# Optimization experiments

Hardware: AMD Instinct MI355X
Metric: run time of the kernel (lower is better)

The kernel has to match this reference:

```python
import jax, jax.numpy as jnp
import numpy as np
from jax import lax

FAST_ITERATIONS = 100
INPUT_DIM = 1024
OUTPUT_DIM = 512
BATCH = 16384


def setup_inputs() -> dict:
    key = jax.random.key(0)
    kx, kw, km = jax.random.split(key, 3)
    x = jax.random.normal(kx, (BATCH, INPUT_DIM), dtype=jnp.float32)
    # Xavier-uniform init for W [output_dim, input_dim]
    limit = float(np.sqrt(6.0 / (INPUT_DIM + OUTPUT_DIM)))
    W = jax.random.uniform(kw, (OUTPUT_DIM, INPUT_DIM), dtype=jnp.float32,
                           minval=-limit, maxval=limit)
    # M is zero at init in the module; use a small random M (spectral radius ~0.45)
    # so the fixed-point iteration is stable and non-trivial.
    M = 0.02 * jax.random.normal(km, (OUTPUT_DIM, OUTPUT_DIM), dtype=jnp.float32)
    return {"x": x, "W": W, "M": M}


def reference(x, W, M):
    # y_init = x @ W.T; then 100 steps of y = Wx - y @ M (all coords use old y)
    Wx = x @ W.T  # [batch, output_dim]

    def step(y, _):
        return Wx - y @ M, None

    y, _ = lax.scan(step, Wx, None, length=FAST_ITERATIONS)
    return y
```

## Files before the change

kernel.cpp:

```cpp
#include <hip/hip_runtime.h>

typedef float f32x4 __attribute__((ext_vector_type(4)));
typedef __bf16 bf16x8 __attribute__((ext_vector_type(8)));
typedef unsigned short u16x4 __attribute__((ext_vector_type(4)));
typedef unsigned short u16x8 __attribute__((ext_vector_type(8)));

__device__ __forceinline__ unsigned short f2b(float f){
  return __builtin_bit_cast(unsigned short, (__bf16)f);
}
__device__ __forceinline__ float b2f(unsigned short u){
  union { unsigned x; float f; } v; v.x = ((unsigned)u) << 16; return v.f;
}
__device__ __forceinline__ void mfma3(f32x4& acc, bf16x8 ah, bf16x8 al, bf16x8 bh, bf16x8 bl){
  acc = __builtin_amdgcn_mfma_f32_16x16x32_bf16(ah, bh, acc, 0, 0, 0);
  acc = __builtin_amdgcn_mfma_f32_16x16x32_bf16(ah, bl, acc, 0, 0, 0);
  acc = __builtin_amdgcn_mfma_f32_16x16x32_bf16(al, bh, acc, 0, 0, 0);
}
__device__ __forceinline__ void gload16(const void* g, void* l){
  __builtin_amdgcn_global_load_lds((const __attribute__((address_space(1))) void*)g,
                                   (__attribute__((address_space(3))) void*)l, 16, 0, 0);
}

template<bool ATR>
__device__ __forceinline__ void loadA(const float* __restrict__ A, int i0, int k0,
                                      int tid, float* aR){
  if (ATR){
    int r32 = tid & 31, kg = tid >> 5;
    #pragma unroll
    for (int q = 0; q < 8; ++q)
      aR[q] = -A[(k0 + kg*8 + q)*512 + i0 + r32];
  } else {
    #pragma unroll
    for (int j = 0; j < 2; ++j){
      int p = tid + j*256;
      int row = p >> 4, kq = p & 15;
      f32x4 v = *reinterpret_cast<const f32x4*>(A + (i0+row)*512 + k0 + kq*4);
      #pragma unroll
      for (int e = 0; e < 4; ++e) aR[j*4+e] = v[e];
    }
  }
}
template<bool ATR>
__device__ __forceinline__ void writeA(const float* aR, int tid,
                                       unsigned short* Ah, unsigned short* Al){
  if (ATR){
    int r32 = tid & 31, kg = tid >> 5;
    #pragma unroll
    for (int q4 = 0; q4 < 2; ++q4){
      u16x4 hi, lo;
      #pragma unroll
      for (int e = 0; e < 4; ++e){
        float f = aR[q4*4+e];
        unsigned short h = f2b(f);
        hi[e] = h; lo[e] = f2b(f - b2f(h));
      }
      int off = r32*128 + (((kg*8 + q4*4)*2) ^ ((r32 & 7) << 4));
      *reinterpret_cast<u16x4*>((char*)Ah + off) = hi;
      *reinterpret_cast<u16x4*>((char*)Al + off) = lo;
    }
  } else {
    #pragma unroll
    for (int j = 0; j < 2; ++j){
      int p = tid + j*256;
      int row = p >> 4, kq = p & 15;
      u16x4 hi, lo;
      #pragma unroll
      for (int e = 0; e < 4; ++e){
        float f = aR[j*4+e];
        unsigned short h = f2b(f);
        hi[e] = h; lo[e] = f2b(f - b2f(h));
      }
      int off = row*128 + ((kq*8) ^ ((row & 7) << 4));
      *reinterpret_cast<u16x4*>((char*)Ah + off) = hi;
      *reinterpret_cast<u16x4*>((char*)Al + off) = lo;
    }
  }
}
template<bool BROWM>
__device__ __forceinline__ void loadB(const float* __restrict__ B, int j0, int k0,
                                      int sb, int tid, float* bR){
  if (BROWM){
    #pragma unroll
    for (int j = 0; j < 4; ++j){
      int p = tid + j*256;
      int n = p >> 4, kq = p & 15;
      f32x4 v = *reinterpret_cast<const f32x4*>(B + (j0+n)*512 + k0 + kq*4);
      #pragma unroll
      for (int e = 0; e < 4; ++e) bR[j*4+e] = -v[e];
    }
  } else {
    int n = tid & 63, kg = tid >> 6;
    #pragma unroll
    for (int q = 0; q < 16; ++q)
      bR[q] = B[(k0 + kg*16 + q)*sb + j0 + n];
  }
}
template<bool BROWM>
__device__ __forceinline__ void writeB(const float* bR, int tid,
                                       unsigned short* Bh, unsigned short* Bl){
  if (BROWM){
    #pragma unroll
    for (int j = 0; j < 4; ++j){
      int p = tid + j*256;
      int n = p >> 4, kq = p & 15;
      u16x4 hi, lo;
      #pragma unroll
      for (int e = 0; e < 4; ++e){
        float f = bR[j*4+e];
        unsigned short h = f2b(f);
        hi[e] = h; lo[e] = f2b(f - b2f(h));
      }
      int off = n*128 + ((kq*8) ^ ((n & 7) << 4));
      *reinterpret_cast<u16x4*>((char*)Bh + off) = hi;
      *reinterpret_cast<u16x4*>((char*)Bl + off) = lo;
    }
  } else {
    int n = tid & 63, kg = tid >> 6;
    #pragma unroll
    for (int q4 = 0; q4 < 4; ++q4){
      u16x4 hi, lo;
      #pragma unroll
      for (int e = 0; e < 4; ++e){
        float f = bR[q4*4+e];
        unsigned short h = f2b(f);
        hi[e] = h; lo[e] = f2b(f - b2f(h));
      }
      int off = n*128 + (((kg*16 + q4*4)*2) ^ ((n & 7) << 4));
      *reinterpret_cast<u16x4*>((char*)Bh + off) = hi;
      *reinterpret_cast<u16x4*>((char*)Bl + off) = lo;
    }
  }
}

template<bool ATR, bool BROWM, bool HASD, bool BFOUT>
__device__ __forceinline__ void gtile(
    const float* __restrict__ A, const float* __restrict__ B,
    const float* __restrict__ D, float* __restrict__ Cf,
    unsigned short* __restrict__ Cb, int i0, int j0, int sb, int so,
    unsigned short* Ah, unsigned short* Al,
    unsigned short* Bh, unsigned short* Bl, int tid)
{
  int lane = tid & 63, wave = tid >> 6;
  int wm = wave >> 1, wn = wave & 1;
  f32x4 acc[2] = {};
  float aR0[8], bR0[16], aR1[8], bR1[16];
  loadA<ATR>(A, i0, 0, tid, aR0);
  loadB<BROWM>(B, j0, 0, sb, tid, bR0);
  loadA<ATR>(A, i0, 64, tid, aR1);
  loadB<BROWM>(B, j0, 64, sb, tid, bR1);

#define CHAIN_MFMA_PHASE                                                   \
    { _Pragma("unroll")                                                    \
      for (int kk = 0; kk < 2; ++kk){                                      \
        int kb = (kk*32 + (lane >> 4)*8) * 2;                              \
        int arow = wm*16 + (lane & 15);                                    \
        int aoff = arow*128 + (kb ^ ((arow & 7) << 4));                    \
        bf16x8 ah = *reinterpret_cast<const bf16x8*>((char*)Ah + aoff);    \
        bf16x8 al = *reinterpret_cast<const bf16x8*>((char*)Al + aoff);    \
        _Pragma("unroll")                                                  \
        for (int n = 0; n < 2; ++n){                                       \
          int brow = wn*32 + n*16 + (lane & 15);                           \
          int boff = brow*128 + (kb ^ ((brow & 7) << 4));                  \
          bf16x8 bh = *reinterpret_cast<const bf16x8*>((char*)Bh + boff);  \
          bf16x8 bl = *reinterpret_cast<const bf16x8*>((char*)Bl + boff);  \
          mfma3(acc[n], ah, al, bh, bl);                                   \
        }                                                                  \
      } }

  #pragma unroll 1
  for (int k0 = 0; k0 < 512; k0 += 128){
    writeA<ATR>(aR0, tid, Ah, Al);
    writeB<BROWM>(bR0, tid, Bh, Bl);
    __syncthreads();
    if (k0 + 128 < 512){
      loadA<ATR>(A, i0, k0 + 128, tid, aR0);
      loadB<BROWM>(B, j0, k0 + 128, sb, tid, bR0);
    }
    CHAIN_MFMA_PHASE
    __syncthreads();
    writeA<ATR>(aR1, tid, Ah, Al);
    writeB<BROWM>(bR1, tid, Bh, Bl);
    __syncthreads();
    if (k0 + 192 < 512){
      loadA<ATR>(A, i0, k0 + 192, tid, aR1);
      loadB<BROWM>(B, j0, k0 + 192, sb, tid, bR1);
    }
    CHAIN_MFMA_PHASE
    __syncthreads();
  }
#undef CHAIN_MFMA_PHASE

  #pragma unroll
  for (int n = 0; n < 2; ++n)
    #pragma unroll
    for (int r = 0; r < 4; ++r){
      int i = i0 + wm*16 + (lane >> 4)*4 + r;
      int j = j0 + wn*32 + n*16 + (lane & 15);
      float v = acc[n][r];
      if (HASD) v += D[i*so + j];
      if (BFOUT) Cb[i*so + j] = f2b(v);
      else       Cf[i*so + j] = v;
    }
}

__global__ __launch_bounds__(256, 2) void k_step(
    const float* __restrict__ Q, const float* __restrict__ R,
    float* __restrict__ Qout, float* __restrict__ Rout,
    unsigned short* __restrict__ Tout,
    const float* __restrict__ X, unsigned short* __restrict__ Xb,
    int first, int last, int convbase, int convend)
{
  __shared__ unsigned short Ah[32*64], Al[32*64], Bh[64*64], Bl[64*64];
  int tid = threadIdx.x, bid = blockIdx.x;
  int qend = last ? 256 : 384;
  if (bid < 256){
    int i0 = (bid >> 4) * 32, j0 = (bid & 15) * 64;
    if (last)
      gtile<false,false,true ,true >(Q, R, R, nullptr, Tout, i0, j0, 1024, 1024, Ah,Al,Bh,Bl, tid);
    else if (first)
      gtile<true ,false,true ,false>(Q, R, R, Rout, nullptr, i0, j0, 1024, 1024, Ah,Al,Bh,Bl, tid);
    else
      gtile<false,false,true ,false>(Q, R, R, Rout, nullptr, i0, j0, 1024, 1024, Ah,Al,Bh,Bl, tid);
  } else if (bid < qend){
    int t = bid - 256;
    int i0 = (t >> 3) * 32, j0 = (t & 7) * 64;
    if (first)
      gtile<true ,true ,false,false>(Q, Q, nullptr, Qout, nullptr, i0, j0, 512, 512, Ah,Al,Bh,Bl, tid);
    else
      gtile<false,false,false,false>(Q, Q, nullptr, Qout, nullptr, i0, j0, 512, 512, Ah,Al,Bh,Bl, tid);
  } else {
    for (int g = convbase + (bid - qend); g < convend; g += 128){
      const float* src = X + (size_t)g * 8192;
      unsigned short* dst = Xb + (size_t)g * 8192;
      #pragma unroll
      for (int it = 0; it < 8; ++it){
        int p = (tid + it*256) * 4;
        f32x4 v = *reinterpret_cast<const f32x4*>(src + p);
        u16x4 h;
        #pragma unroll
        for (int e = 0; e < 4; ++e) h[e] = f2b(v[e]);
        *reinterpret_cast<u16x4*>(dst + p) = h;
      }
    }
  }
}

__global__ __launch_bounds__(512, 1) void k_gemm10(const unsigned short* __restrict__ Xb,
                                                   const unsigned short* __restrict__ Tt,
                                                   float* __restrict__ Y)
{
  __shared__ unsigned short As_[2][128*64];
  __shared__ unsigned short Bs_[2][256*64];
  int tid = threadIdx.x;
  int lane = tid & 63, wave = tid >> 6;
  int wm = wave >> 2, wn = wave & 3;
  int bid = blockIdx.x;
  int wg = (bid & 7) * 32 + (bid >> 3);
  int m0 = (wg >> 1) * 128;
  int n0 = (wg & 1) * 256;

  int lrow = lane >> 3;
  int lg   = (lane & 7) ^ lrow;
  f32x4 acc[4][4] = {};

  #define STAGE(buf, kt)                                                         \
    { _Pragma("unroll")                                                          \
      for (int it = 0; it < 2; ++it){                                            \
        int r = wave*16 + it*8 + lrow;                                           \
        gload16((const void*)(Xb + (size_t)(m0 + r)*1024 + (kt)*64 + lg*8),      \
                (void*)&As_[buf][(wave*16 + it*8)*64]);                          \
      }                                                                          \
      _Pragma("unroll")                                                          \
      for (int it = 0; it < 4; ++it){                                            \
        int r = wave*32 + it*8 + lrow;                                           \
        gload16((const void*)(Tt + (size_t)(n0 + r)*1024 + (kt)*64 + lg*8),      \
                (void*)&Bs_[buf][(wave*32 + it*8)*64]);                          \
      } }

  STAGE(0, 0);
  STAGE(1, 1);
  #pragma unroll 1
  for (int kt = 0; kt < 16; ++kt){
    if (kt < 15) asm volatile("s_waitcnt vmcnt(6)" ::: "memory");
    else         asm volatile("s_waitcnt vmcnt(0)" ::: "memory");
    __builtin_amdgcn_s_barrier();
    const unsigned short* Ab = &As_[kt & 1][0];
    const unsigned short* Bb = &Bs_[kt & 1][0];
    #pragma unroll
    for (int kk = 0; kk < 2; ++kk){
      int gb = kk*4 + (lane >> 4);
      bf16x8 af[4], bfr[4];
      #pragma unroll
      for (int m = 0; m < 4; ++m){
        int row = wm*64 + m*16 + (lane & 15);
        af[m] = *reinterpret_cast<const bf16x8*>((char*)Ab + row*128 + ((gb ^ (row & 7))*16));
      }
      #pragma unroll
      for (int n = 0; n < 4; ++n){
        int row = wn*64 + n*16 + (lane & 15);
        bfr[n] = *reinterpret_cast<const bf16x8*>((char*)Bb + row*128 + ((gb ^ (row & 7))*16));
      }
      #pragma unroll
      for (int m = 0; m < 4; ++m)
        #pragma unroll
        for (int n = 0; n < 4; ++n)
          acc[m][n] = __builtin_amdgcn_mfma_f32_16x16x32_bf16(af[m], bfr[n], acc[m][n], 0,0,0);
    }
    __builtin_amdgcn_s_barrier();
    if (kt < 14) STAGE(kt & 1, kt + 2);
  }
  #undef STAGE

  #pragma unroll
  for (int m = 0; m < 4; ++m)
    #pragma unroll
    for (int n = 0; n < 4; ++n)
      #pragma unroll
      for (int r = 0; r < 4; ++r){
        int row = m0 + wm*64 + m*16 + (lane >> 4)*4 + r;
        int col = n0 + wn*64 + n*16 + (lane & 15);
        Y[(size_t)row*512 + col] = acc[m][n][r];
      }
}

extern "C" void kernel_launch(void* const* d_in, const int* in_sizes, int n_in,
                              void* d_out, int out_size, void* d_ws, size_t ws_size,
                              hipStream_t stream) {
  const float* x = (const float*)d_in[0];
  const float* W = (const float*)d_in[1];
  const float* M = (const float*)d_in[2];
  float* y = (float*)d_out;

  float* Qa = (float*)d_ws;
  float* Qb = Qa + 512*512;
  float* Ra = Qb + 512*512;
  float* Rb = Ra + 512*1024;
  unsigned short* Tt = (unsigned short*)(Rb + 512*1024);
  unsigned short* Xb = Tt + 512*1024;

  k_step<<<512, 256, 0, stream>>>(M,  W,  Qa, Ra, nullptr, x, Xb, 1, 0,    0,  512);
  k_step<<<512, 256, 0, stream>>>(Qa, Ra, Qb, Rb, nullptr, x, Xb, 0, 0,  512, 1024);
  k_step<<<512, 256, 0, stream>>>(Qb, Rb, Qa, Ra, nullptr, x, Xb, 0, 0, 1024, 1536);
  k_step<<<384, 256, 0, stream>>>(Qa, Ra, nullptr, nullptr, Tt, x, Xb, 0, 1, 1536, 2048);
  k_gemm10<<<256, 512, 0, stream>>>(Xb, Tt, y);
}
```

Before: 73.07 us.

## Triple-buffer final GEMM, reshape tile to 256x128, interleave loads with MFMA

Reworks the final bf16 GEMM kernel to use three LDS buffers instead of two, which removes the trailing barrier. The next-next stage's global-to-LDS loads are issued between the fragment reads and the MFMA bursts, split between the two k-halves. The block tile changes from 128x256 to 256x128 with a 4x2 wave layout, and s_setprio raises wave priority around the MFMA bursts. The aim is better overlap of memory traffic with compute, at the cost of more LDS use and a buffer-reuse scheme that depends on the vmcnt and barrier ordering being correct.

```diff
diff --git a/kernel.cpp b/kernel.cpp
--- a/kernel.cpp
+++ b/kernel.cpp
@@ -245,50 +245,55 @@
   }
 }
 
-__global__ __launch_bounds__(512, 1) void k_gemm10(const unsigned short* __restrict__ Xb,
+__global__ __launch_bounds__(512, 1) void k_gemm14(const unsigned short* __restrict__ Xb,
                                                    const unsigned short* __restrict__ Tt,
                                                    float* __restrict__ Y)
 {
-  __shared__ unsigned short As_[2][128*64];
-  __shared__ unsigned short Bs_[2][256*64];
+  __shared__ unsigned short As_[3][256*64];
+  __shared__ unsigned short Bs_[3][128*64];
   int tid = threadIdx.x;
   int lane = tid & 63, wave = tid >> 6;
-  int wm = wave >> 2, wn = wave & 3;
+  int wm = wave >> 1, wn = wave & 1;
   int bid = blockIdx.x;
   int wg = (bid & 7) * 32 + (bid >> 3);
-  int m0 = (wg >> 1) * 128;
-  int n0 = (wg & 1) * 256;
+  int m0 = (wg >> 2) * 256;
+  int n0 = (wg & 3) * 128;
 
   int lrow = lane >> 3;
   int lg   = (lane & 7) ^ lrow;
   f32x4 acc[4][4] = {};
 
-  #define STAGE(buf, kt)                                                         \
+  #define STAGE_A(buf, kt)                                                       \
+    { _Pragma("unroll")                                                          \
+      for (int it = 0; it < 4; ++it){                                            \
+        int r = wave*32 + it*8 + lrow;                                           \
+        gload16((const void*)(Xb + (size_t)(m0 + r)*1024 + (kt)*64 + lg*8),      \
+                (void*)&As_[buf][(wave*32 + it*8)*64]);                          \
+      } }
+  #define STAGE_B(buf, kt)                                                       \
     { _Pragma("unroll")                                                          \
       for (int it = 0; it < 2; ++it){                                            \
         int r = wave*16 + it*8 + lrow;                                           \
-        gload16((const void*)(Xb + (size_t)(m0 + r)*1024 + (kt)*64 + lg*8),      \
-                (void*)&As_[buf][(wave*16 + it*8)*64]);                          \
-      }                                                                          \
-      _Pragma("unroll")                                                          \
-      for (int it = 0; it < 4; ++it){                                            \
-        int r = wave*32 + it*8 + lrow;                                           \
         gload16((const void*)(Tt + (size_t)(n0 + r)*1024 + (kt)*64 + lg*8),      \
-                (void*)&Bs_[buf][(wave*32 + it*8)*64]);                          \
+                (void*)&Bs_[buf][(wave*16 + it*8)*64]);                          \
       } }
 
-  STAGE(0, 0);
-  STAGE(1, 1);
+  STAGE_A(0, 0); STAGE_B(0, 0);
+  STAGE_A(1, 1); STAGE_B(1, 1);
+
+  int buf = 0;
   #pragma unroll 1
   for (int kt = 0; kt < 16; ++kt){
     if (kt < 15) asm volatile("s_waitcnt vmcnt(6)" ::: "memory");
     else         asm volatile("s_waitcnt vmcnt(0)" ::: "memory");
     __builtin_amdgcn_s_barrier();
-    const unsigned short* Ab = &As_[kt & 1][0];
-    const unsigned short* Bb = &Bs_[kt & 1][0];
-    #pragma unroll
-    for (int kk = 0; kk < 2; ++kk){
-      int gb = kk*4 + (lane >> 4);
+    const unsigned short* Ab = &As_[buf][0];
+    const unsigned short* Bb = &Bs_[buf][0];
+    int nbuf = buf + 1; if (nbuf == 3) nbuf = 0;
+    int sbuf = nbuf + 1; if (sbuf == 3) sbuf = 0;
+
+    {
+      int gb = (lane >> 4);
       bf16x8 af[4], bfr[4];
       #pragma unroll
       for (int m = 0; m < 4; ++m){
@@ -300,16 +305,41 @@
         int row = wn*64 + n*16 + (lane & 15);
         bfr[n] = *reinterpret_cast<const bf16x8*>((char*)Bb + row*128 + ((gb ^ (row & 7))*16));
       }
+      if (kt < 14) STAGE_A(sbuf, kt + 2);
+      __builtin_amdgcn_s_setprio(1);
       #pragma unroll
       for (int m = 0; m < 4; ++m)
         #pragma unroll
         for (int n = 0; n < 4; ++n)
           acc[m][n] = __builtin_amdgcn_mfma_f32_16x16x32_bf16(af[m], bfr[n], acc[m][n], 0,0,0);
-    }
-    __builtin_amdgcn_s_barrier();
-    if (kt < 14) STAGE(kt & 1, kt + 2);
-  }
-  #undef STAGE
+      __builtin_amdgcn_s_setprio(0);
+    }
+    {
+      int gb = 4 + (lane >> 4);
+      bf16x8 af[4], bfr[4];
+      #pragma unroll
+      for (int m = 0; m < 4; ++m){
+        int row = wm*64 + m*16 + (lane & 15);
+        af[m] = *reinterpret_cast<const bf16x8*>((char*)Ab + row*128 + ((gb ^ (row & 7))*16));
+      }
+      #pragma unroll
+      for (int n = 0; n < 4; ++n){
+        int row = wn*64 + n*16 + (lane & 15);
+        bfr[n] = *reinterpret_cast<const bf16x8*>((char*)Bb + row*128 + ((gb ^ (row & 7))*16));
+      }
+      if (kt < 14) STAGE_B(sbuf, kt + 2);
+      __builtin_amdgcn_s_setprio(1);
+      #pragma unroll
+      for (int m = 0; m < 4; ++m)
+        #pragma unroll
+        for (int n = 0; n < 4; ++n)
+          acc[m][n] = __builtin_amdgcn_mfma_f32_16x16x32_bf16(af[m], bfr[n], acc[m][n], 0,0,0);
+      __builtin_amdgcn_s_setprio(0);
+    }
+    buf = nbuf;
+  }
+  #undef STAGE_A
+  #undef STAGE_B
 
   #pragma unroll
   for (int m = 0; m < 4; ++m)
@@ -342,5 +372,5 @@
   k_step<<<512, 256, 0, stream>>>(Qa, Ra, Qb, Rb, nullptr, x, Xb, 0, 0,  512, 1024);
   k_step<<<512, 256, 0, stream>>>(Qb, Rb, Qa, Ra, nullptr, x, Xb, 0, 0, 1024, 1536);
   k_step<<<384, 256, 0, stream>>>(Qa, Ra, nullptr, nullptr, Tt, x, Xb, 0, 1, 1536, 2048);
-  k_gemm10<<<256, 512, 0, stream>>>(Xb, Tt, y);
-}
+  k_gemm14<<<256, 512, 0, stream>>>(Xb, Tt, y);
+}
```

Result: faster. 70.28 us (-3.8%).
